# Kernel optimization log

Hardware: AMD Instinct MI355X
Metric: run time of the kernel (lower is better)

The kernel has to match this reference:

```python
import jax, jax.numpy as jnp
import numpy as np

N = 100_000      # nodes per type
E = 1_000_000    # edges per edge type
F_IN = 32        # raw feature dim
HID = 64         # hidden_channels
H, D = 2, 32     # num_heads, head_dim


def setup_inputs() -> dict:
    key = jax.random.key(0)
    ks = jax.random.split(key, 64)
    it = iter(range(64))
    def nrm(shape, scale=0.1):
        return jax.random.normal(ks[next(it)], shape, dtype=jnp.float32) * scale
    inp = {}
    inp['x_mac'] = jax.random.normal(ks[next(it)], (N, F_IN), dtype=jnp.float32)
    inp['x_buf'] = jax.random.normal(ks[next(it)], (N, F_IN), dtype=jnp.float32)
    inp['ei_m2b'] = jax.random.randint(ks[next(it)], (2, E), 0, N)
    inp['ei_b2m'] = jax.random.randint(ks[next(it)], (2, E), 0, N)
    for t in ('mac', 'buf'):
        inp[f'enc_w_{t}'] = nrm((F_IN, HID))
        inp[f'enc_b_{t}'] = jnp.zeros((HID,), jnp.float32)
        inp[f'enc_g_{t}'] = jnp.ones((HID,), jnp.float32)
        inp[f'enc_be_{t}'] = jnp.zeros((HID,), jnp.float32)
        for p in ('k', 'q', 'v'):
            inp[f'{p}_w_{t}'] = nrm((HID, HID))
            inp[f'{p}_b_{t}'] = jnp.zeros((HID,), jnp.float32)
        inp[f'o_w_{t}'] = nrm((HID, HID))
        inp[f'o_b_{t}'] = jnp.zeros((HID,), jnp.float32)
        inp[f'skip_{t}'] = jnp.ones((), jnp.float32)
    for r in ('m2b', 'b2m'):
        inp[f'a_{r}'] = nrm((H, D, D))
        inp[f'm_{r}'] = nrm((H, D, D))
        inp[f'p_{r}'] = jnp.ones((H,), jnp.float32)
    inp['ln_g'] = jnp.ones((HID,), jnp.float32)
    inp['ln_b'] = jnp.zeros((HID,), jnp.float32)
    return inp


def _ln(x, g, b, eps=1e-5):
    mu = jnp.mean(x, -1, keepdims=True)
    var = jnp.mean((x - mu) ** 2, -1, keepdims=True)
    return g * (x - mu) * jax.lax.rsqrt(var + eps) + b


def _seg_softmax(logits, seg, n):
    # logits: [E, H], seg: [E] dst ids. Numerically stable per-segment softmax.
    m = jax.ops.segment_max(logits, seg, num_segments=n)
    m = jnp.where(jnp.isfinite(m), m, 0.0)  # empty segments -> -inf
    e = jnp.exp(logits - m[seg])
    s = jax.ops.segment_sum(e, seg, num_segments=n)
    return e / (s[seg] + 1e-16)


def _hgt_edge(q_dst, k_src, v_src, a_rel, m_rel, p_rel, ei, n_dst):
    # q_dst:[Nd,H,D] k_src/v_src:[Ns,H,D] a_rel/m_rel:[H,D,D] p_rel:[H] ei:[2,E]
    src, dst = ei[0], ei[1]
    k = jnp.einsum('nhd,hde->nhe', k_src, a_rel)   # relation-transform keys
    v = jnp.einsum('nhd,hde->nhe', v_src, m_rel)   # relation-transform values
    alpha = (q_dst[dst] * k[src]).sum(-1) * p_rel / jnp.sqrt(jnp.float32(D))  # [E,H]
    alpha = _seg_softmax(alpha, dst, n_dst)
    msg = v[src] * alpha[..., None]                # [E,H,D]
    return jax.ops.segment_sum(msg, dst, num_segments=n_dst).reshape(n_dst, H * D)


def _forward(x_mac, x_buf, ei_m2b, ei_b2m,
             enc_w_mac, enc_b_mac, enc_g_mac, enc_be_mac,
             enc_w_buf, enc_b_buf, enc_g_buf, enc_be_buf,
             k_w_mac, k_b_mac, q_w_mac, q_b_mac, v_w_mac, v_b_mac,
             k_w_buf, k_b_buf, q_w_buf, q_b_buf, v_w_buf, v_b_buf,
             o_w_mac, o_b_mac, o_w_buf, o_b_buf, skip_mac, skip_buf,
             a_m2b, m_m2b, p_m2b, a_b2m, m_b2m, p_b2m, ln_g, ln_b):
    n_mac, n_buf = x_mac.shape[0], x_buf.shape[0]
    # per-type encoder: Linear -> LayerNorm -> ReLU (dropout = identity in eval)
    h_mac = jax.nn.relu(_ln(x_mac @ enc_w_mac + enc_b_mac, enc_g_mac, enc_be_mac))
    h_buf = jax.nn.relu(_ln(x_buf @ enc_w_buf + enc_b_buf, enc_g_buf, enc_be_buf))
    # HGTConv: per-type k/q/v projections -> [N,H,D]
    k_mac = (h_mac @ k_w_mac + k_b_mac).reshape(n_mac, H, D)
    q_mac = (h_mac @ q_w_mac + q_b_mac).reshape(n_mac, H, D)
    v_mac = (h_mac @ v_w_mac + v_b_mac).reshape(n_mac, H, D)
    k_buf = (h_buf @ k_w_buf + k_b_buf).reshape(n_buf, H, D)
    q_buf = (h_buf @ q_w_buf + q_b_buf).reshape(n_buf, H, D)
    v_buf = (h_buf @ v_w_buf + v_b_buf).reshape(n_buf, H, D)
    # per-edge-type attention + scatter-softmax + sum aggregate
    agg_buf = _hgt_edge(q_buf, k_mac, v_mac, a_m2b, m_m2b, p_m2b, ei_m2b, n_buf)
    agg_mac = _hgt_edge(q_mac, k_buf, v_buf, a_b2m, m_b2m, p_b2m, ei_b2m, n_mac)
    # per-dst-type output: out_lin(gelu(agg)), sigmoid-skip gating with input
    a_mac = jax.nn.gelu(agg_mac, approximate=False) @ o_w_mac + o_b_mac
    a_buf = jax.nn.gelu(agg_buf, approximate=False) @ o_w_buf + o_b_buf
    g_mac = jax.nn.sigmoid(skip_mac)
    g_buf = jax.nn.sigmoid(skip_buf)
    conv_mac = g_mac * a_mac + (1.0 - g_mac) * h_mac
    conv_buf = g_buf * a_buf + (1.0 - g_buf) * h_buf
    # module-level residual + shared LayerNorm
    y_mac = _ln(conv_mac + h_mac, ln_g, ln_b)
    y_buf = _ln(conv_buf + h_buf, ln_g, ln_b)
    return y_mac, y_buf


def reference(x_mac, x_buf, ei_m2b, ei_b2m,
              enc_w_mac, enc_b_mac, enc_g_mac, enc_be_mac,
              enc_w_buf, enc_b_buf, enc_g_buf, enc_be_buf,
              k_w_mac, k_b_mac, q_w_mac, q_b_mac, v_w_mac, v_b_mac,
              k_w_buf, k_b_buf, q_w_buf, q_b_buf, v_w_buf, v_b_buf,
              o_w_mac, o_b_mac, o_w_buf, o_b_buf, skip_mac, skip_buf,
              a_m2b, m_m2b, p_m2b, a_b2m, m_b2m, p_b2m, ln_g, ln_b):
    return _forward(x_mac, x_buf, ei_m2b, ei_b2m,
                    enc_w_mac, enc_b_mac, enc_g_mac, enc_be_mac,
                    enc_w_buf, enc_b_buf, enc_g_buf, enc_be_buf,
                    k_w_mac, k_b_mac, q_w_mac, q_b_mac, v_w_mac, v_b_mac,
                    k_w_buf, k_b_buf, q_w_buf, q_b_buf, v_w_buf, v_b_buf,
                    o_w_mac, o_b_mac, o_w_buf, o_b_buf, skip_mac, skip_buf,
                    a_m2b, m_m2b, p_m2b, a_b2m, m_b2m, p_b2m, ln_g, ln_b)
```

## Files before the change

kernel.cpp:

```cpp
#include <hip/hip_runtime.h>
#include <hip/hip_bf16.h>
#include <math.h>

#define NN 100000
#define NN2 200000
#define NE 1000000
#define FIN 32
#define HIDC 64

#define NB 782
#define NBP 1024
#define EPB 4096
#define SCGRID 489
#define CAP 3072
#define MAXIT 12
#define KQV_BLKS 1563
#define NPOS 12

typedef unsigned int u32;
typedef unsigned short u16;

typedef __attribute__((ext_vector_type(8))) short bf16x8;
typedef __attribute__((ext_vector_type(4))) float f32x4;
typedef __attribute__((ext_vector_type(2))) float f32x2;

__device__ __forceinline__ float wsum(float v) {
  #pragma unroll
  for (int off = 32; off; off >>= 1) v += __shfl_xor(v, off, 64);
  return v;
}

__device__ __forceinline__ u16 f2bf(float f) {
  union { float f; u32 u; } c; c.f = f;
  u32 u = c.u;
  return (u16)((u + 0x7FFFu + ((u >> 16) & 1u)) >> 16);
}

__device__ __forceinline__ float bf2f(u32 v) {
  union { u32 u; float f; } c; c.u = v << 16; return c.f;
}

__device__ __forceinline__ bf16x8 ldfrag(const u16* p) {
  uint4 v = *(const uint4*)p;
  union { uint4 u; bf16x8 b; } c; c.u = v; return c.b;
}

__device__ __forceinline__ void scan1024(u32* a, u32* wtot) {
  int t = threadIdx.x, lane = t & 63, wv = t >> 6;
  u32 v0 = a[t * 4 + 0], v1 = a[t * 4 + 1], v2 = a[t * 4 + 2], v3 = a[t * 4 + 3];
  u32 sum = v0 + v1 + v2 + v3;
  u32 x = sum;
  #pragma unroll
  for (int off = 1; off < 64; off <<= 1) {
    u32 y = __shfl_up(x, off, 64);
    if (lane >= off) x += y;
  }
  if (lane == 63) wtot[wv] = x;
  u32 excl = x - sum;
  __syncthreads();
  u32 wb = 0;
  #pragma unroll
  for (int w = 0; w < 4; w++) if (w < wv) wb += wtot[w];
  u32 b = wb + excl;
  a[t * 4 + 0] = b;
  a[t * 4 + 1] = b + v0;
  a[t * 4 + 2] = b + v0 + v1;
  a[t * 4 + 3] = b + v0 + v1 + v2;
}

__device__ __forceinline__ void edge_decode(
    int ee, const int* __restrict__ ei_m2b, const int* __restrict__ ei_b2m,
    int& src_g, int& dst_g) {
  if (ee < NE) {
    src_g = ei_m2b[ee];
    dst_g = NN + ei_m2b[NE + ee];
  } else {
    int e2 = ee - NE;
    src_g = NN + ei_b2m[e2];
    dst_g = ei_b2m[NE + e2];
  }
}

#define FUSE2_T (192 * 64 + 192)
__global__ __launch_bounds__(256) void k_fuse2(
    const float* __restrict__ qw0, const float* __restrict__ qb0,
    const float* __restrict__ kw0, const float* __restrict__ kb0,
    const float* __restrict__ vw0, const float* __restrict__ vb0,
    const float* __restrict__ ar0, const float* __restrict__ mr0,
    const float* __restrict__ p0,
    const float* __restrict__ qw1, const float* __restrict__ qb1,
    const float* __restrict__ kw1, const float* __restrict__ kb1,
    const float* __restrict__ vw1, const float* __restrict__ vb1,
    const float* __restrict__ ar1, const float* __restrict__ mr1,
    const float* __restrict__ p1,
    u16* __restrict__ WfTb, float* __restrict__ bfv,
    u32* __restrict__ gcursor) {
  int gidx = blockIdx.x * 256 + threadIdx.x;
  if (gidx < NBP) gcursor[gidx] = 0;
  if (gidx >= 2 * FUSE2_T) return;
  int type = gidx >= FUSE2_T;
  int idx = gidx - type * FUSE2_T;
  const float* qw = type ? qw1 : qw0; const float* qb = type ? qb1 : qb0;
  const float* kw = type ? kw1 : kw0; const float* kb = type ? kb1 : kb0;
  const float* vw = type ? vw1 : vw0; const float* vb = type ? vb1 : vb0;
  const float* ar = type ? ar1 : ar0; const float* mr = type ? mr1 : mr0;
  const float* p  = type ? p1  : p0;
  if (idx < 192 * 64) {
    int c = idx >> 6, k = idx & 63;
    float o;
    if (c < 64) {
      o = qw[k * 64 + c];
    } else {
      int e = c & 63, hd = e >> 5, ee = e & 31;
      bool isK = c < 128;
      const float* M = isK ? ar : mr;
      const float* Wsrc = isK ? kw : vw;
      float s = 0.0f;
      #pragma unroll
      for (int d = 0; d < 32; ++d)
        s += Wsrc[k * 64 + hd * 32 + d] * M[hd * 32 * 32 + d * 32 + ee];
      if (isK) s *= p[hd] * 0.17677669529663687f;
      o = s;
    }
    WfTb[(size_t)type * 192 * 64 + c * 64 + k] = f2bf(o);
  } else {
    int c = idx - 192 * 64;
    float o;
    if (c < 64) {
      o = qb[c];
    } else {
      int e = c & 63, hd = e >> 5, ee = e & 31;
      bool isK = c < 128;
      const float* M = isK ? ar : mr;
      const float* Bb = isK ? kb : vb;
      float s = 0.0f;
      #pragma unroll
      for (int d = 0; d < 32; ++d)
        s += Bb[hd * 32 + d] * M[hd * 32 * 32 + d * 32 + ee];
      if (isK) s *= p[hd] * 0.17677669529663687f;
      o = s;
    }
    bfv[(size_t)type * 192 + c] = o;
  }
}

__global__ __launch_bounds__(256) void k_enc3(
    const float* __restrict__ x_mac, const float* __restrict__ x_buf,
    const float* __restrict__ w_mac, const float* __restrict__ b_mac,
    const float* __restrict__ g_mac, const float* __restrict__ be_mac,
    const float* __restrict__ w_buf, const float* __restrict__ b_buf,
    const float* __restrict__ g_buf, const float* __restrict__ be_buf,
    u16* __restrict__ hb) {
  __shared__ float xs[64][FIN + 1];
  __shared__ float ts[64][HIDC + 1];
  int t = threadIdx.x;
  int b = blockIdx.x;
  int type = b >= KQV_BLKS;
  int r0   = type ? (NN + (b - KQV_BLKS) * 64) : (b * 64);
  int rend = type ? NN2 : NN;
  const float* w  = type ? w_buf  : w_mac;
  const float* bb = type ? b_buf  : b_mac;
  const float* g  = type ? g_buf  : g_mac;
  const float* be = type ? be_buf : be_mac;
  const float* x  = type ? x_buf  : x_mac;
  int xoff = type ? NN : 0;
  for (int i = t; i < 64 * 8; i += 256) {
    int row = i >> 3, c4 = i & 7;
    int gr = r0 + row; if (gr >= rend) gr = rend - 1;
    float4 v = *(const float4*)&x[(size_t)(gr - xoff) * FIN + c4 * 4];
    xs[row][c4 * 4 + 0] = v.x; xs[row][c4 * 4 + 1] = v.y;
    xs[row][c4 * 4 + 2] = v.z; xs[row][c4 * 4 + 3] = v.w;
  }
  __syncthreads();
  int rg = t & 15, cg = t >> 4;
  float acc[4][4];
  #pragma unroll
  for (int c = 0; c < 4; c++) {
    float bv = bb[cg * 4 + c];
    #pragma unroll
    for (int r = 0; r < 4; r++) acc[r][c] = bv;
  }
  for (int k = 0; k < FIN; ++k) {
    float a0 = xs[rg * 4 + 0][k];
    float a1 = xs[rg * 4 + 1][k];
    float a2 = xs[rg * 4 + 2][k];
    float a3 = xs[rg * 4 + 3][k];
    float4 wv4 = *(const float4*)&w[k * HIDC + cg * 4];
    acc[0][0] = fmaf(a0, wv4.x, acc[0][0]); acc[0][1] = fmaf(a0, wv4.y, acc[0][1]);
    acc[0][2] = fmaf(a0, wv4.z, acc[0][2]); acc[0][3] = fmaf(a0, wv4.w, acc[0][3]);
    acc[1][0] = fmaf(a1, wv4.x, acc[1][0]); acc[1][1] = fmaf(a1, wv4.y, acc[1][1]);
    acc[1][2] = fmaf(a1, wv4.z, acc[1][2]); acc[1][3] = fmaf(a1, wv4.w, acc[1][3]);
    acc[2][0] = fmaf(a2, wv4.x, acc[2][0]); acc[2][1] = fmaf(a2, wv4.y, acc[2][1]);
    acc[2][2] = fmaf(a2, wv4.z, acc[2][2]); acc[2][3] = fmaf(a2, wv4.w, acc[2][3]);
    acc[3][0] = fmaf(a3, wv4.x, acc[3][0]); acc[3][1] = fmaf(a3, wv4.y, acc[3][1]);
    acc[3][2] = fmaf(a3, wv4.z, acc[3][2]); acc[3][3] = fmaf(a3, wv4.w, acc[3][3]);
  }
  #pragma unroll
  for (int r = 0; r < 4; r++)
    #pragma unroll
    for (int c = 0; c < 4; c++) ts[rg * 4 + r][cg * 4 + c] = acc[r][c];
  __syncthreads();
  int wv = t >> 6, ln = t & 63;
  for (int rr = wv; rr < 64; rr += 4) {
    int gr = r0 + rr;
    if (gr >= rend) break;
    float v = ts[rr][ln];
    float mu = wsum(v) * (1.0f / HIDC);
    float d = v - mu;
    float var = wsum(d * d) * (1.0f / HIDC);
    float yv = g[ln] * d * rsqrtf(var + 1e-5f) + be[ln];
    hb[(size_t)gr * HIDC + ln] = f2bf(fmaxf(yv, 0.0f));
  }
}

__global__ __launch_bounds__(256) void k_kqv5(
    const u16* __restrict__ hb, const u16* __restrict__ WfTb,
    const float* __restrict__ bfv,
    u32* __restrict__ qp, u32* __restrict__ kvt8) {
  int t = threadIdx.x;
  int b = blockIdx.x;
  int type = b >= KQV_BLKS;
  int r0   = type ? (NN + (b - KQV_BLKS) * 64) : (b * 64);
  int rend = type ? NN2 : NN;
  const u16* WT = WfTb + (size_t)type * 192 * 64;
  const float* B = bfv + (size_t)type * 192;
  int w = t >> 6, l = t & 63;
  int lr = l & 15, lk = l >> 4;
  int arow = r0 + w * 16 + lr;
  int arowc = arow >= rend ? rend - 1 : arow;
  bf16x8 a0 = ldfrag(&hb[(size_t)arowc * 64 + lk * 8]);
  bf16x8 a1 = ldfrag(&hb[(size_t)arowc * 64 + 32 + lk * 8]);
  f32x4 acc[12];
  #pragma unroll
  for (int j = 0; j < 12; j++) {
    bf16x8 b0 = ldfrag(&WT[(size_t)(j * 16 + lr) * 64 + lk * 8]);
    bf16x8 b1 = ldfrag(&WT[(size_t)(j * 16 + lr) * 64 + 32 + lk * 8]);
    f32x4 c = {0.0f, 0.0f, 0.0f, 0.0f};
    c = __builtin_amdgcn_mfma_f32_16x16x32_bf16(a0, b0, c, 0, 0, 0);
    c = __builtin_amdgcn_mfma_f32_16x16x32_bf16(a1, b1, c, 0, 0, 0);
    acc[j] = c;
  }
  int orow0 = r0 + w * 16 + lk * 4;
  float bq0 = B[lr],       bq1 = B[16 + lr],  bq2 = B[32 + lr],  bq3 = B[48 + lr];
  float bk0 = B[64 + lr],  bk1 = B[80 + lr],  bk2 = B[96 + lr],  bk3 = B[112 + lr];
  float bv0 = B[128 + lr], bv1 = B[144 + lr], bv2 = B[160 + lr], bv3 = B[176 + lr];
  #pragma unroll
  for (int r = 0; r < 4; ++r) {
    int orow = orow0 + r;
    if (orow >= rend) break;
    u32 w0 = (u32)f2bf(acc[0][r] + bq0) | ((u32)f2bf(acc[2][r] + bq2) << 16);
    u32 w1 = (u32)f2bf(acc[1][r] + bq1) | ((u32)f2bf(acc[3][r] + bq3) << 16);
    qp[(size_t)orow * 32 + lr]      = w0;
    qp[(size_t)orow * 32 + 16 + lr] = w1;
    int p0 = __builtin_amdgcn_cvt_pk_fp8_f32(acc[4][r] + bk0, acc[8][r] + bv0, 0, false);
    p0     = __builtin_amdgcn_cvt_pk_fp8_f32(acc[6][r] + bk2, acc[10][r] + bv2, p0, true);
    int p1 = __builtin_amdgcn_cvt_pk_fp8_f32(acc[5][r] + bk1, acc[9][r] + bv1, 0, false);
    p1     = __builtin_amdgcn_cvt_pk_fp8_f32(acc[7][r] + bk3, acc[11][r] + bv3, p1, true);
    kvt8[(size_t)orow * 32 + lr]      = (u32)p0;
    kvt8[(size_t)orow * 32 + 16 + lr] = (u32)p1;
  }
}

__global__ __launch_bounds__(256) void k_out3(
    const u16* __restrict__ aggb, const u16* __restrict__ hb,
    const float* __restrict__ ow0, const float* __restrict__ ob0,
    const float* __restrict__ skip0,
    const float* __restrict__ ow1, const float* __restrict__ ob1,
    const float* __restrict__ skip1,
    const float* __restrict__ lg, const float* __restrict__ lb,
    float* __restrict__ y) {
  __shared__ float gs[64][65];
  int t = threadIdx.x;
  int b = blockIdx.x;
  int type = b >= KQV_BLKS;
  int r0   = type ? (NN + (b - KQV_BLKS) * 64) : (b * 64);
  int rend = type ? NN2 : NN;
  const float* ow = type ? ow1 : ow0;
  const float* ob = type ? ob1 : ob0;
  float gk = 1.0f / (1.0f + expf(-(type ? skip1 : skip0)[0]));
  for (int i = t; i < 64 * 8; i += 256) {
    int row = i >> 3, c8 = i & 7;
    int gr = r0 + row; if (gr >= rend) gr = rend - 1;
    uint4 v = *(const uint4*)&aggb[(size_t)gr * 64 + c8 * 8];
    u32 a[4] = { v.x, v.y, v.z, v.w };
    #pragma unroll
    for (int j = 0; j < 4; j++) {
      float f0 = bf2f(a[j] & 0xFFFFu);
      float f1 = bf2f(a[j] >> 16);
      gs[row][c8 * 8 + j * 2]     = 0.5f * f0 * (1.0f + erff(f0 * 0.70710678118654752f));
      gs[row][c8 * 8 + j * 2 + 1] = 0.5f * f1 * (1.0f + erff(f1 * 0.70710678118654752f));
    }
  }
  __syncthreads();
  int rg = t & 15, cg = t >> 4;
  float acc[4][4];
  #pragma unroll
  for (int c = 0; c < 4; c++) {
    float bv = ob[cg * 4 + c];
    #pragma unroll
    for (int r = 0; r < 4; r++) acc[r][c] = bv;
  }
  for (int k = 0; k < 64; ++k) {
    float a0 = gs[rg * 4 + 0][k];
    float a1 = gs[rg * 4 + 1][k];
    float a2 = gs[rg * 4 + 2][k];
    float a3 = gs[rg * 4 + 3][k];
    float4 wv4 = *(const float4*)&ow[k * 64 + cg * 4];
    acc[0][0] = fmaf(a0, wv4.x, acc[0][0]); acc[0][1] = fmaf(a0, wv4.y, acc[0][1]);
    acc[0][2] = fmaf(a0, wv4.z, acc[0][2]); acc[0][3] = fmaf(a0, wv4.w, acc[0][3]);
    acc[1][0] = fmaf(a1, wv4.x, acc[1][0]); acc[1][1] = fmaf(a1, wv4.y, acc[1][1]);
    acc[1][2] = fmaf(a1, wv4.z, acc[1][2]); acc[1][3] = fmaf(a1, wv4.w, acc[1][3]);
    acc[2][0] = fmaf(a2, wv4.x, acc[2][0]); acc[2][1] = fmaf(a2, wv4.y, acc[2][1]);
    acc[2][2] = fmaf(a2, wv4.z, acc[2][2]); acc[2][3] = fmaf(a2, wv4.w, acc[2][3]);
    acc[3][0] = fmaf(a3, wv4.x, acc[3][0]); acc[3][1] = fmaf(a3, wv4.y, acc[3][1]);
    acc[3][2] = fmaf(a3, wv4.z, acc[3][2]); acc[3][3] = fmaf(a3, wv4.w, acc[3][3]);
  }
  float tv[4][4];
  float c2 = 2.0f - gk;
  #pragma unroll
  for (int r = 0; r < 4; r++) {
    int gr = r0 + rg * 4 + r; if (gr >= rend) gr = rend - 1;
    uint2 hv = *(const uint2*)&hb[(size_t)gr * 64 + cg * 4];
    float h0 = bf2f(hv.x & 0xFFFFu), h1 = bf2f(hv.x >> 16);
    float h2 = bf2f(hv.y & 0xFFFFu), h3 = bf2f(hv.y >> 16);
    tv[r][0] = fmaf(gk, acc[r][0], c2 * h0);
    tv[r][1] = fmaf(gk, acc[r][1], c2 * h1);
    tv[r][2] = fmaf(gk, acc[r][2], c2 * h2);
    tv[r][3] = fmaf(gk, acc[r][3], c2 * h3);
  }
  __syncthreads();
  #pragma unroll
  for (int r = 0; r < 4; r++)
    #pragma unroll
    for (int c = 0; c < 4; c++) gs[rg * 4 + r][cg * 4 + c] = tv[r][c];
  __syncthreads();
  int wv = t >> 6, ln = t & 63;
  for (int rr = wv; rr < 64; rr += 4) {
    int gr = r0 + rr;
    if (gr >= rend) break;
    float v = gs[rr][ln];
    float mu = wsum(v) * (1.0f / HIDC);
    float d = v - mu;
    float var = wsum(d * d) * (1.0f / HIDC);
    y[(size_t)gr * HIDC + ln] = lg[ln] * d * rsqrtf(var + 1e-5f) + lb[ln];
  }
}

__global__ __launch_bounds__(256) void k_bscatter2(
    const int* __restrict__ ei_m2b, const int* __restrict__ ei_b2m,
    u32* __restrict__ gcursor, u32* __restrict__ bpairs) {
  __shared__ u32 hist[NBP];
  __shared__ u32 loff[NBP];
  __shared__ u32 gbase[NBP];
  __shared__ u32 wtot[4];
  __shared__ u32 pairs[EPB];
  __shared__ u16 sbuck[EPB];
  int tid = threadIdx.x;
  for (int i = tid; i < NBP; i += 256) hist[i] = 0;
  __syncthreads();
  int base_e = blockIdx.x * EPB;
  u32 pk[EPB / 256];
  u16 bk[EPB / 256];
  u16 rk[EPB / 256];
  #pragma unroll
  for (int i = 0; i < EPB / 256; i++) {
    int ee = base_e + i * 256 + tid;
    if (ee < 2 * NE) {
      int src_g, dst_g;
      edge_decode(ee, ei_m2b, ei_b2m, src_g, dst_g);
      u32 b = (u32)dst_g >> 8;
      pk[i] = ((u32)(dst_g & 255) << 18) | (u32)src_g;
      bk[i] = (u16)b;
      rk[i] = (u16)atomicAdd(&hist[b], 1u);
    } else {
      bk[i] = 0xFFFFu;
    }
  }
  __syncthreads();
  for (int i = tid; i < NBP; i += 256) loff[i] = hist[i];
  __syncthreads();
  scan1024(loff, wtot);
  __syncthreads();
  #pragma unroll
  for (int i = 0; i < EPB / 256; i++) {
    if (bk[i] != 0xFFFFu) {
      u32 s = loff[bk[i]] + rk[i];
      pairs[s] = pk[i];
      sbuck[s] = bk[i];
    }
  }
  __syncthreads();
  for (int b = tid; b < NBP; b += 256) {
    u32 c = hist[b];
    gbase[b] = c ? atomicAdd(&gcursor[b], c) : 0u;
  }
  __syncthreads();
  int nval = 2 * NE - base_e;
  if (nval > EPB) nval = EPB;
  for (int s = tid; s < nval; s += 256) {
    u32 b = sbuck[s];
    u32 slot = gbase[b] + (s - loff[b]);
    if (slot < CAP) bpairs[(size_t)b * CAP + slot] = pairs[s];
  }
}

#define EDGE_STEP(W) {                                                        \
    f32x2 x0 = __builtin_amdgcn_cvt_pk_f32_fp8((int)W.x, false);              \
    f32x2 x1 = __builtin_amdgcn_cvt_pk_f32_fp8((int)W.x, true);               \
    f32x2 y0 = __builtin_amdgcn_cvt_pk_f32_fp8((int)W.y, false);              \
    f32x2 y1 = __builtin_amdgcn_cvt_pk_f32_fp8((int)W.y, true);               \
    float p0 = fmaf(q1, y0.x, q0 * x0.x);                                     \
    float p1 = fmaf(qh1, y1.x, qh0 * x1.x);                                   \
    p0 += __shfl_xor(p0, 1, 64); p1 += __shfl_xor(p1, 1, 64);                 \
    p0 += __shfl_xor(p0, 2, 64); p1 += __shfl_xor(p1, 2, 64);                 \
    p0 += __shfl_xor(p0, 4, 64); p1 += __shfl_xor(p1, 4, 64);                 \
    p0 += __shfl_xor(p0, 8, 64); p1 += __shfl_xor(p1, 8, 64);                 \
    float mn0 = fmaxf(m0, p0);                                                \
    float c0 = __expf(m0 - mn0);                                              \
    float w0 = __expf(p0 - mn0);                                              \
    s0 = fmaf(s0, c0, w0);                                                    \
    va00 = fmaf(va00, c0, w0 * x0.y);                                         \
    va01 = fmaf(va01, c0, w0 * y0.y);                                         \
    m0 = mn0;                                                                 \
    float mn1 = fmaxf(m1, p1);                                                \
    float c1 = __expf(m1 - mn1);                                              \
    float w1 = __expf(p1 - mn1);                                              \
    s1 = fmaf(s1, c1, w1);                                                    \
    va10 = fmaf(va10, c1, w1 * x1.y);                                         \
    va11 = fmaf(va11, c1, w1 * y1.y);                                         \
    m1 = mn1;                                                                 \
  }

__global__ __launch_bounds__(256) void k_bedge7(
    const u32* __restrict__ gcursor, const u32* __restrict__ bpairs,
    const u32* __restrict__ qp, const u32* __restrict__ kvt8,
    u16* __restrict__ aggb) {
  __shared__ u32 srt[CAP];
  __shared__ u32 hist[64];
  __shared__ u32 rowptr[65];
  int tid = threadIdx.x;
  int b = blockIdx.x >> 2;
  u32 qr = blockIdx.x & 3;
  u32 cnt = gcursor[b];
  int n = (int)(cnt > CAP ? CAP : cnt);
  if (tid < 64) hist[tid] = 0;
  __syncthreads();
  u32 pk[MAXIT];
  #pragma unroll
  for (int it = 0; it < MAXIT; it++) {
    pk[it] = 0xFFFFFFFFu;
    int i = tid + it * 256;
    if (i < n) {
      u32 p = bpairs[(size_t)b * CAP + i];
      u32 ld = p >> 18;
      if ((ld >> 6) == qr) {
        atomicAdd(&hist[ld & 63], 1u);
        pk[it] = p;
      }
    }
  }
  __syncthreads();
  if (tid < 64) {
    u32 v = hist[tid];
    u32 x = v;
    #pragma unroll
    for (int off = 1; off < 64; off <<= 1) {
      u32 y = __shfl_up(x, off, 64);
      if (tid >= off) x += y;
    }
    rowptr[tid] = x - v;
    if (tid == 63) rowptr[64] = x;
  }
  __syncthreads();
  if (tid < 64) hist[tid] = rowptr[tid];
  __syncthreads();
  #pragma unroll
  for (int it = 0; it < MAXIT; it++) {
    u32 p = pk[it];
    if (p != 0xFFFFFFFFu) {
      u32 pos = atomicAdd(&hist[(p >> 18) & 63], 1u);
      srt[pos] = p & 0x3FFFFu;
    }
  }
  __syncthreads();
  {
    int sd = tid >> 2, sub = tid & 3;
    u32 sj0 = rowptr[sd], sj1 = rowptr[sd + 1];
    u32 kk[NPOS]; u32 rr[NPOS]; int np = 0;
    for (u32 p = sj0 + sub; p < sj1; p += 4) {
      u32 key = srt[p];
      u32 rank = sj0;
      for (u32 q = sj0; q < sj1; ++q) {
        u32 v = srt[q];
        rank += (v < key) || (v == key && q < p);
      }
      if (np < NPOS) { kk[np] = key; rr[np] = rank; np++; }
    }
    __syncthreads();
    for (int i = 0; i < np; ++i) srt[rr[i]] = kk[i];
  }
  __syncthreads();
  int grp = tid >> 4, t = tid & 15;
  for (int ld = grp; ld < 64; ld += 16) {
    int dst_g = (b << 8) + ((int)qr << 6) + ld;
    if (dst_g >= NN2) continue;
    u32 j0 = rowptr[ld], j1 = rowptr[ld + 1];
    uint2 qp2 = *(const uint2*)&qp[(size_t)dst_g * 32 + 2 * t];
    float q0  = bf2f(qp2.x & 0xFFFFu);
    float qh0 = bf2f(qp2.x >> 16);
    float q1  = bf2f(qp2.y & 0xFFFFu);
    float qh1 = bf2f(qp2.y >> 16);
    float m0 = -1e30f, s0 = 0.0f, m1 = -1e30f, s1 = 0.0f;
    float va00 = 0.0f, va01 = 0.0f, va10 = 0.0f, va11 = 0.0f;
    u32 j = j0;
    for (; j + 2 <= j1; j += 2) {
      u32 sA = srt[j], sB = srt[j + 1];
      uint2 wA = *(const uint2*)&kvt8[(size_t)sA * 32 + 2 * t];
      uint2 wB = *(const uint2*)&kvt8[(size_t)sB * 32 + 2 * t];
      EDGE_STEP(wA); EDGE_STEP(wB);
    }
    if (j < j1) {
      u32 sA = srt[j];
      uint2 wA = *(const uint2*)&kvt8[(size_t)sA * 32 + 2 * t];
      EDGE_STEP(wA);
    }
    float inv0 = 1.0f / (s0 + 1e-16f);
    float inv1 = 1.0f / (s1 + 1e-16f);
    u32 o0 = (u32)f2bf(va00 * inv0) | ((u32)f2bf(va01 * inv0) << 16);
    u32 o1 = (u32)f2bf(va10 * inv1) | ((u32)f2bf(va11 * inv1) << 16);
    *(u32*)&aggb[(size_t)dst_g * 64 + 2 * t]      = o0;
    *(u32*)&aggb[(size_t)dst_g * 64 + 32 + 2 * t] = o1;
  }
}

extern "C" void kernel_launch(void* const* d_in, const int* in_sizes, int n_in,
                              void* d_out, int out_size, void* d_ws, size_t ws_size,
                              hipStream_t stream) {
  const float* x_mac     = (const float*)d_in[0];
  const float* x_buf     = (const float*)d_in[1];
  const int*   ei_m2b    = (const int*)d_in[2];
  const int*   ei_b2m    = (const int*)d_in[3];
  const float* enc_w_mac = (const float*)d_in[4];
  const float* enc_b_mac = (const float*)d_in[5];
  const float* enc_g_mac = (const float*)d_in[6];
  const float* enc_be_mac= (const float*)d_in[7];
  const float* k_w_mac   = (const float*)d_in[8];
  const float* k_b_mac   = (const float*)d_in[9];
  const float* q_w_mac   = (const float*)d_in[10];
  const float* q_b_mac   = (const float*)d_in[11];
  const float* v_w_mac   = (const float*)d_in[12];
  const float* v_b_mac   = (const float*)d_in[13];
  const float* o_w_mac   = (const float*)d_in[14];
  const float* o_b_mac   = (const float*)d_in[15];
  const float* skip_mac  = (const float*)d_in[16];
  const float* enc_w_buf = (const float*)d_in[17];
  const float* enc_b_buf = (const float*)d_in[18];
  const float* enc_g_buf = (const float*)d_in[19];
  const float* enc_be_buf= (const float*)d_in[20];
  const float* k_w_buf   = (const float*)d_in[21];
  const float* k_b_buf   = (const float*)d_in[22];
  const float* q_w_buf   = (const float*)d_in[23];
  const float* q_b_buf   = (const float*)d_in[24];
  const float* v_w_buf   = (const float*)d_in[25];
  const float* v_b_buf   = (const float*)d_in[26];
  const float* o_w_buf   = (const float*)d_in[27];
  const float* o_b_buf   = (const float*)d_in[28];
  const float* skip_buf  = (const float*)d_in[29];
  const float* a_m2b     = (const float*)d_in[30];
  const float* m_m2b     = (const float*)d_in[31];
  const float* p_m2b     = (const float*)d_in[32];
  const float* a_b2m     = (const float*)d_in[33];
  const float* m_b2m     = (const float*)d_in[34];
  const float* p_b2m     = (const float*)d_in[35];
  const float* ln_g      = (const float*)d_in[36];
  const float* ln_b      = (const float*)d_in[37];

  char* ws = (char*)d_ws;
  size_t off = 0;
  auto take = [&](size_t bytes) -> char* {
    char* p = ws + off;
    off = (off + bytes + 255) & ~(size_t)255;
    return p;
  };
  u16*   hb      = (u16*)take((size_t)NN2 * HIDC * 2);
  u16*   aggb    = (u16*)take((size_t)NN2 * HIDC * 2);
  u32*   qp      = (u32*)take((size_t)NN2 * 32 * 4);
  u32*   kvt8    = (u32*)take((size_t)NN2 * 32 * 4);
  u16*   WfTb    = (u16*)take((size_t)2 * 192 * 64 * 2);
  float* bfv     = (float*)take((size_t)2 * 192 * 4);
  u32*   gcursor = (u32*)take((size_t)NBP * 4);
  u32*   bpairs  = (u32*)take((size_t)NB * CAP * 4);

  const int tile_grid  = 2 * KQV_BLKS;
  const int fuse2_grid = (2 * FUSE2_T + 255) / 256;

  k_fuse2<<<fuse2_grid, 256, 0, stream>>>(
      q_w_mac, q_b_mac, k_w_mac, k_b_mac, v_w_mac, v_b_mac, a_m2b, m_m2b, p_m2b,
      q_w_buf, q_b_buf, k_w_buf, k_b_buf, v_w_buf, v_b_buf, a_b2m, m_b2m, p_b2m,
      WfTb, bfv, gcursor);
  k_bscatter2<<<SCGRID, 256, 0, stream>>>(ei_m2b, ei_b2m, gcursor, bpairs);
  k_enc3<<<tile_grid, 256, 0, stream>>>(
      x_mac, x_buf,
      enc_w_mac, enc_b_mac, enc_g_mac, enc_be_mac,
      enc_w_buf, enc_b_buf, enc_g_buf, enc_be_buf, hb);
  k_kqv5<<<tile_grid, 256, 0, stream>>>(hb, WfTb, bfv, qp, kvt8);
  k_bedge7<<<4 * NB, 256, 0, stream>>>(gcursor, bpairs, qp, kvt8, aggb);
  k_out3<<<tile_grid, 256, 0, stream>>>(
      aggb, hb, o_w_mac, o_b_mac, skip_mac, o_w_buf, o_b_buf, skip_buf,
      ln_g, ln_b, (float*)d_out);
}
```

Measured before the change: 280.7 us.

## Relayout Q and K/V so each lane holds four dims of one head

Changes the Q output from interleaved packed pairs to a plain row-major bf16 layout. K/V fp8 words are repacked with a neighbour-lane shuffle so each edge-kernel lane owns four consecutive dims of a single head. The edge loop then keeps one online-softmax state per lane instead of two and needs three shuffle-reduction steps instead of four. The price is extra shuffles and half-idle lanes during the K/V store in the projection kernel, and narrower 2-byte Q stores.

New measurement: 272.4 us. -3.0%, faster.

```diff
diff --git a/kernel.cpp b/kernel.cpp
--- a/kernel.cpp
+++ b/kernel.cpp
@@ -213,10 +213,10 @@
   }
 }
 
-__global__ __launch_bounds__(256) void k_kqv5(
+__global__ __launch_bounds__(256) void k_kqv6(
     const u16* __restrict__ hb, const u16* __restrict__ WfTb,
     const float* __restrict__ bfv,
-    u32* __restrict__ qp, u32* __restrict__ kvt8) {
+    u16* __restrict__ qo, u32* __restrict__ kvt8) {
   int t = threadIdx.x;
   int b = blockIdx.x;
   int type = b >= KQV_BLKS;
@@ -241,23 +241,33 @@
     acc[j] = c;
   }
   int orow0 = r0 + w * 16 + lk * 4;
-  float bq0 = B[lr],       bq1 = B[16 + lr],  bq2 = B[32 + lr],  bq3 = B[48 + lr];
-  float bk0 = B[64 + lr],  bk1 = B[80 + lr],  bk2 = B[96 + lr],  bk3 = B[112 + lr];
-  float bv0 = B[128 + lr], bv1 = B[144 + lr], bv2 = B[160 + lr], bv3 = B[176 + lr];
-  #pragma unroll
-  for (int r = 0; r < 4; ++r) {
-    int orow = orow0 + r;
-    if (orow >= rend) break;
-    u32 w0 = (u32)f2bf(acc[0][r] + bq0) | ((u32)f2bf(acc[2][r] + bq2) << 16);
-    u32 w1 = (u32)f2bf(acc[1][r] + bq1) | ((u32)f2bf(acc[3][r] + bq3) << 16);
-    qp[(size_t)orow * 32 + lr]      = w0;
-    qp[(size_t)orow * 32 + 16 + lr] = w1;
-    int p0 = __builtin_amdgcn_cvt_pk_fp8_f32(acc[4][r] + bk0, acc[8][r] + bv0, 0, false);
-    p0     = __builtin_amdgcn_cvt_pk_fp8_f32(acc[6][r] + bk2, acc[10][r] + bv2, p0, true);
-    int p1 = __builtin_amdgcn_cvt_pk_fp8_f32(acc[5][r] + bk1, acc[9][r] + bv1, 0, false);
-    p1     = __builtin_amdgcn_cvt_pk_fp8_f32(acc[7][r] + bk3, acc[11][r] + bv3, p1, true);
-    kvt8[(size_t)orow * 32 + lr]      = (u32)p0;
-    kvt8[(size_t)orow * 32 + 16 + lr] = (u32)p1;
+  #pragma unroll
+  for (int j = 0; j < 4; j++) {
+    float bv = B[j * 16 + lr];
+    #pragma unroll
+    for (int r = 0; r < 4; r++) {
+      int orow = orow0 + r;
+      if (orow < rend)
+        qo[(size_t)orow * 64 + j * 16 + lr] = f2bf(acc[j][r] + bv);
+    }
+  }
+  #pragma unroll
+  for (int j = 0; j < 4; j++) {
+    float bk = B[64 + j * 16 + lr];
+    float bv2 = B[128 + j * 16 + lr];
+    #pragma unroll
+    for (int r = 0; r < 4; r++) {
+      float kt_own = acc[4 + j][r] + bk;
+      float vt_own = acc[8 + j][r] + bv2;
+      float kt_nbr = __shfl_xor(kt_own, 1, 64);
+      float vt_nbr = __shfl_xor(vt_own, 1, 64);
+      int orow = orow0 + r;
+      if (((lr & 1) == 0) && orow < rend) {
+        int pk = __builtin_amdgcn_cvt_pk_fp8_f32(kt_own, vt_own, 0, false);
+        pk     = __builtin_amdgcn_cvt_pk_fp8_f32(kt_nbr, vt_nbr, pk, true);
+        kvt8[(size_t)orow * 32 + (j * 16 + lr) / 2] = (u32)pk;
+      }
+    }
   }
 }
 
@@ -405,35 +415,28 @@
 }
 
 #define EDGE_STEP(W) {                                                        \
-    f32x2 x0 = __builtin_amdgcn_cvt_pk_f32_fp8((int)W.x, false);              \
-    f32x2 x1 = __builtin_amdgcn_cvt_pk_f32_fp8((int)W.x, true);               \
-    f32x2 y0 = __builtin_amdgcn_cvt_pk_f32_fp8((int)W.y, false);              \
-    f32x2 y1 = __builtin_amdgcn_cvt_pk_f32_fp8((int)W.y, true);               \
-    float p0 = fmaf(q1, y0.x, q0 * x0.x);                                     \
-    float p1 = fmaf(qh1, y1.x, qh0 * x1.x);                                   \
-    p0 += __shfl_xor(p0, 1, 64); p1 += __shfl_xor(p1, 1, 64);                 \
-    p0 += __shfl_xor(p0, 2, 64); p1 += __shfl_xor(p1, 2, 64);                 \
-    p0 += __shfl_xor(p0, 4, 64); p1 += __shfl_xor(p1, 4, 64);                 \
-    p0 += __shfl_xor(p0, 8, 64); p1 += __shfl_xor(p1, 8, 64);                 \
-    float mn0 = fmaxf(m0, p0);                                                \
-    float c0 = __expf(m0 - mn0);                                              \
-    float w0 = __expf(p0 - mn0);                                              \
-    s0 = fmaf(s0, c0, w0);                                                    \
-    va00 = fmaf(va00, c0, w0 * x0.y);                                         \
-    va01 = fmaf(va01, c0, w0 * y0.y);                                         \
-    m0 = mn0;                                                                 \
-    float mn1 = fmaxf(m1, p1);                                                \
-    float c1 = __expf(m1 - mn1);                                              \
-    float w1 = __expf(p1 - mn1);                                              \
-    s1 = fmaf(s1, c1, w1);                                                    \
-    va10 = fmaf(va10, c1, w1 * x1.y);                                         \
-    va11 = fmaf(va11, c1, w1 * y1.y);                                         \
-    m1 = mn1;                                                                 \
-  }
-
-__global__ __launch_bounds__(256) void k_bedge7(
+    f32x2 e0 = __builtin_amdgcn_cvt_pk_f32_fp8((int)W.x, false);              \
+    f32x2 e1 = __builtin_amdgcn_cvt_pk_f32_fp8((int)W.x, true);               \
+    f32x2 e2 = __builtin_amdgcn_cvt_pk_f32_fp8((int)W.y, false);              \
+    f32x2 e3 = __builtin_amdgcn_cvt_pk_f32_fp8((int)W.y, true);               \
+    float prod = fmaf(q3, e3.x, fmaf(q2, e2.x, fmaf(q1, e1.x, q0 * e0.x)));   \
+    prod += __shfl_xor(prod, 1, 64);                                          \
+    prod += __shfl_xor(prod, 2, 64);                                          \
+    prod += __shfl_xor(prod, 4, 64);                                          \
+    float mn = fmaxf(m, prod);                                                \
+    float cc = __expf(m - mn);                                                \
+    float we = __expf(prod - mn);                                             \
+    s = fmaf(s, cc, we);                                                      \
+    a0 = fmaf(a0, cc, we * e0.y);                                             \
+    a1 = fmaf(a1, cc, we * e1.y);                                             \
+    a2 = fmaf(a2, cc, we * e2.y);                                             \
+    a3 = fmaf(a3, cc, we * e3.y);                                             \
+    m = mn;                                                                   \
+  }
+
+__global__ __launch_bounds__(256) void k_bedge8(
     const u32* __restrict__ gcursor, const u32* __restrict__ bpairs,
-    const u32* __restrict__ qp, const u32* __restrict__ kvt8,
+    const u16* __restrict__ q, const u32* __restrict__ kvt8,
     u16* __restrict__ aggb) {
   __shared__ u32 srt[CAP];
   __shared__ u32 hist[64];
@@ -490,9 +493,9 @@
     for (u32 p = sj0 + sub; p < sj1; p += 4) {
       u32 key = srt[p];
       u32 rank = sj0;
-      for (u32 q = sj0; q < sj1; ++q) {
-        u32 v = srt[q];
-        rank += (v < key) || (v == key && q < p);
+      for (u32 qq = sj0; qq < sj1; ++qq) {
+        u32 v = srt[qq];
+        rank += (v < key) || (v == key && qq < p);
       }
       if (np < NPOS) { kk[np] = key; rr[np] = rank; np++; }
     }
@@ -505,13 +508,11 @@
     int dst_g = (b << 8) + ((int)qr << 6) + ld;
     if (dst_g >= NN2) continue;
     u32 j0 = rowptr[ld], j1 = rowptr[ld + 1];
-    uint2 qp2 = *(const uint2*)&qp[(size_t)dst_g * 32 + 2 * t];
-    float q0  = bf2f(qp2.x & 0xFFFFu);
-    float qh0 = bf2f(qp2.x >> 16);
-    float q1  = bf2f(qp2.y & 0xFFFFu);
-    float qh1 = bf2f(qp2.y >> 16);
-    float m0 = -1e30f, s0 = 0.0f, m1 = -1e30f, s1 = 0.0f;
-    float va00 = 0.0f, va01 = 0.0f, va10 = 0.0f, va11 = 0.0f;
+    uint2 qp2 = *(const uint2*)&q[(size_t)dst_g * 64 + t * 4];
+    float q0 = bf2f(qp2.x & 0xFFFFu), q1 = bf2f(qp2.x >> 16);
+    float q2 = bf2f(qp2.y & 0xFFFFu), q3 = bf2f(qp2.y >> 16);
+    float m = -1e30f, s = 0.0f;
+    float a0 = 0.0f, a1 = 0.0f, a2 = 0.0f, a3 = 0.0f;
     u32 j = j0;
     for (; j + 2 <= j1; j += 2) {
       u32 sA = srt[j], sB = srt[j + 1];
@@ -524,12 +525,11 @@
       uint2 wA = *(const uint2*)&kvt8[(size_t)sA * 32 + 2 * t];
       EDGE_STEP(wA);
     }
-    float inv0 = 1.0f / (s0 + 1e-16f);
-    float inv1 = 1.0f / (s1 + 1e-16f);
-    u32 o0 = (u32)f2bf(va00 * inv0) | ((u32)f2bf(va01 * inv0) << 16);
-    u32 o1 = (u32)f2bf(va10 * inv1) | ((u32)f2bf(va11 * inv1) << 16);
-    *(u32*)&aggb[(size_t)dst_g * 64 + 2 * t]      = o0;
-    *(u32*)&aggb[(size_t)dst_g * 64 + 32 + 2 * t] = o1;
+    float inv = 1.0f / (s + 1e-16f);
+    u32 o0 = (u32)f2bf(a0 * inv) | ((u32)f2bf(a1 * inv) << 16);
+    u32 o1 = (u32)f2bf(a2 * inv) | ((u32)f2bf(a3 * inv) << 16);
+    uint2 o = { o0, o1 };
+    *(uint2*)&aggb[(size_t)dst_g * 64 + t * 4] = o;
   }
 }
 
@@ -584,7 +584,7 @@
   };
   u16*   hb      = (u16*)take((size_t)NN2 * HIDC * 2);
   u16*   aggb    = (u16*)take((size_t)NN2 * HIDC * 2);
-  u32*   qp      = (u32*)take((size_t)NN2 * 32 * 4);
+  u16*   q       = (u16*)take((size_t)NN2 * HIDC * 2);
   u32*   kvt8    = (u32*)take((size_t)NN2 * 32 * 4);
   u16*   WfTb    = (u16*)take((size_t)2 * 192 * 64 * 2);
   float* bfv     = (float*)take((size_t)2 * 192 * 4);
@@ -603,8 +603,8 @@
       x_mac, x_buf,
       enc_w_mac, enc_b_mac, enc_g_mac, enc_be_mac,
       enc_w_buf, enc_b_buf, enc_g_buf, enc_be_buf, hb);
-  k_kqv5<<<tile_grid, 256, 0, stream>>>(hb, WfTb, bfv, qp, kvt8);
-  k_bedge7<<<4 * NB, 256, 0, stream>>>(gcursor, bpairs, qp, kvt8, aggb);
+  k_kqv6<<<tile_grid, 256, 0, stream>>>(hb, WfTb, bfv, q, kvt8);
+  k_bedge8<<<4 * NB, 256, 0, stream>>>(gcursor, bpairs, q, kvt8, aggb);
   k_out3<<<tile_grid, 256, 0, stream>>>(
       aggb, hb, o_w_mac, o_b_mac, skip_mac, o_w_buf, o_b_buf, skip_buf,
       ln_g, ln_b, (float*)d_out);
```
